# Performance work log

Measured on AMD Instinct MI355X. Metric: run time of the kernel, lower is better.

## Reference

```python
import jax, jax.numpy as jnp
import numpy as np

B, S, D, H = 2, 2048, 2048, 16
HD = D // H  # head_dim = 128


def setup_inputs() -> dict:
    key = jax.random.key(0)
    ks = jax.random.split(key, 9)
    s = 1.0 / np.sqrt(D)
    return {
        "x": jax.random.normal(ks[0], (B, S, D), jnp.float32),
        "Wq": jax.random.normal(ks[1], (D, D), jnp.float32) * s,
        "bq": jax.random.normal(ks[2], (D,), jnp.float32) * 0.02,
        "Wk": jax.random.normal(ks[3], (D, D), jnp.float32) * s,
        "bk": jax.random.normal(ks[4], (D,), jnp.float32) * 0.02,
        "Wv": jax.random.normal(ks[5], (D, D), jnp.float32) * s,
        "bv": jax.random.normal(ks[6], (D,), jnp.float32) * 0.02,
        "Wo": jax.random.normal(ks[7], (D, D), jnp.float32) * s,
        "bo": jax.random.normal(ks[8], (D,), jnp.float32) * 0.02,
    }


def reference(x, Wq, bq, Wk, bk, Wv, bv, Wo, bo):
    b, s, d = x.shape
    # nn.Linear: y = x @ W.T + b
    def split(t):
        # [b, s, d] -> [b, H, s, HD]
        return t.reshape(b, s, H, HD).transpose(0, 2, 1, 3)

    q = split(x @ Wq.T + bq)
    k = split(x @ Wk.T + bk)
    v = split(x @ Wv.T + bv)

    scale = jnp.asarray(HD, x.dtype) ** 0.5
    qk = jnp.einsum("bhqd,bhkd->bhqk", q, k) / scale  # [b, H, s, s]
    weights = jax.nn.softmax(qk, axis=-1)
    attn = jnp.einsum("bhqk,bhkd->bhqd", weights, v)  # [b, H, s, HD]

    merged = attn.transpose(0, 2, 1, 3).reshape(b, s, d)
    return merged @ Wo.T + bo
```

## Files before the change

### kernel.cpp

```cpp
#include <hip/hip_runtime.h>

typedef __bf16 bf16_t;
typedef bf16_t bf16x8 __attribute__((ext_vector_type(8)));
typedef bf16_t bf16x4 __attribute__((ext_vector_type(4)));
typedef float  f32x4  __attribute__((ext_vector_type(4)));

#define DDIM  2048
#define SEQ   2048
#define NH    16
#define HDIM  128
#define BATCH 2
#define MROWS (BATCH * SEQ)
#define XEL   ((size_t)MROWS * DDIM)
#define WEL   ((size_t)DDIM * DDIM)

__device__ __forceinline__ void async_ld16(const bf16_t* g, bf16_t* l) {
  __builtin_amdgcn_global_load_lds(
      (const __attribute__((address_space(1))) void*)g,
      (__attribute__((address_space(3))) void*)l, 16, 0, 0);
}

__global__ void cvt_all(const float* __restrict__ x,
                        const float* __restrict__ w0,
                        const float* __restrict__ w1,
                        const float* __restrict__ w2,
                        const float* __restrict__ w3,
                        bf16_t* __restrict__ ox, bf16_t* __restrict__ ow) {
  const size_t CX = XEL / 4;
  const size_t CW = WEL / 4;
  const size_t total = CX + 4 * CW;
  size_t c = (size_t)blockIdx.x * blockDim.x + threadIdx.x;
  const size_t stride = (size_t)gridDim.x * blockDim.x;
  for (; c < total; c += stride) {
    float4 v;
    bf16_t* outp;
    if (c < CX) {
      v = reinterpret_cast<const float4*>(x)[c];
      outp = ox + c * 4;
    } else {
      const size_t d = c - CX;
      const size_t seg = d >> 20;
      const float* w = seg == 0 ? w0 : seg == 1 ? w1 : seg == 2 ? w2 : w3;
      v = reinterpret_cast<const float4*>(w)[d & (CW - 1)];
      outp = ow + d * 4;
    }
    bf16x4 o;
    o[0] = (bf16_t)v.x; o[1] = (bf16_t)v.y;
    o[2] = (bf16_t)v.z; o[3] = (bf16_t)v.w;
    *reinterpret_cast<bf16x4*>(outp) = o;
  }
}

#define QMM(NF, BV)                                                           \
  __builtin_amdgcn_s_setprio(1);                                              \
  _Pragma("unroll") for (int mf = 0; mf < 4; ++mf) {                          \
    acc[mf][NF] = __builtin_amdgcn_mfma_f32_16x16x32_bf16(                    \
        a_[mf][0], BV[0], acc[mf][NF], 0, 0, 0);                              \
    acc[mf][NF] = __builtin_amdgcn_mfma_f32_16x16x32_bf16(                    \
        a_[mf][1], BV[1], acc[mf][NF], 0, 0, 0);                              \
  }                                                                           \
  __builtin_amdgcn_s_setprio(0);

#define LGKM(N)                                                               \
  asm volatile("s_waitcnt lgkmcnt(" #N ")" ::: "memory");                     \
  __builtin_amdgcn_sched_barrier(0);

__global__ __launch_bounds__(512, 2) void gemm_qkv(
    const bf16_t* __restrict__ Ax, const bf16_t* __restrict__ Wcat,
    const float* __restrict__ bq, const float* __restrict__ bk,
    const float* __restrict__ bv,
    bf16_t* __restrict__ QKVh, float qscale) {
  __shared__ __align__(16) bf16_t sA[2][2][128 * 64];
  __shared__ __align__(16) bf16_t sB[3][192 * 64];

  const int tid  = threadIdx.x;
  const int lane = tid & 63;
  const int w    = tid >> 6;
  const int wm   = w >> 1;
  const int wn   = w & 1;
  const int lg   = lane >> 4;
  const int lr   = lane & 15;

  const int bid = blockIdx.x;
  const int l   = (bid & 7) * 64 + (bid >> 3);
  const int tm  = l & 15;
  const int tn  = l >> 4;
  const int row0  = tm * 256;
  const int ncol0 = tn * 192;

  auto stA = [&](int buf, int ha, int kt) {
#pragma unroll
    for (int L = 0; L < 2; ++L) {
      const int c = L * 512 + tid, r = c >> 3, ch = c & 7;
      async_ld16(Ax + (size_t)(row0 + ha * 128 + r) * DDIM + kt * 64 +
                     ((ch ^ (r & 7)) * 8),
                 &sA[buf][ha][c * 8]);
    }
  };
  auto stB = [&](int buf, int kt) {
#pragma unroll
    for (int L = 0; L < 3; ++L) {
      const int c = L * 512 + tid, r = c >> 3, ch = c & 7;
      async_ld16(Wcat + (size_t)(ncol0 + r) * DDIM + kt * 64 +
                     ((ch ^ (r & 7)) * 8),
                 &sB[buf][c * 8]);
    }
  };
  auto ldA = [&](int buf, int mf, int k) {
    const int row = (wm & 1) * 64 + mf * 16 + lr;
    const int ch  = (k * 4 + lg) ^ (row & 7);
    return *reinterpret_cast<const bf16x8*>(
        &sA[buf][wm >> 1][row * 64 + ch * 8]);
  };
  auto ldB = [&](int buf, int nf, int k) {
    const int row = wn * 96 + nf * 16 + lr;
    const int ch  = (k * 4 + lg) ^ (row & 7);
    return *reinterpret_cast<const bf16x8*>(&sB[buf][row * 64 + ch * 8]);
  };

  f32x4 acc[4][6] = {};

  stA(0, 0, 0); stA(0, 1, 0);
  stB(0, 0);
  stB(1, 1);
  asm volatile("s_waitcnt vmcnt(3)" ::: "memory");
  __builtin_amdgcn_s_barrier();

  int bc = 0;
  for (int t = 0; t < 32; ++t) {
    const int p   = t & 1;
    const int pn  = p ^ 1;
    const int tn1 = (t + 1) & 31, tn2 = (t + 2) & 31;
    const int b2i = bc == 0 ? 2 : bc - 1;

    bf16x8 a_[4][2];
#pragma unroll
    for (int mf = 0; mf < 4; ++mf) {
      a_[mf][0] = ldA(p, mf, 0);
      a_[mf][1] = ldA(p, mf, 1);
    }
    bf16x8 b0[2], b1[2], b2[2], b3[2], b4[2], b5[2];
    b0[0] = ldB(bc, 0, 0); b0[1] = ldB(bc, 0, 1);
    b1[0] = ldB(bc, 1, 0); b1[1] = ldB(bc, 1, 1);
    b2[0] = ldB(bc, 2, 0); b2[1] = ldB(bc, 2, 1);
    __builtin_amdgcn_sched_barrier(0);
    stA(pn, 0, tn1); stA(pn, 1, tn1);
    stB(b2i, tn2);
    __builtin_amdgcn_sched_barrier(0);
    LGKM(4)
    QMM(0, b0)
    b3[0] = ldB(bc, 3, 0); b3[1] = ldB(bc, 3, 1);
    __builtin_amdgcn_sched_barrier(0);
    LGKM(4)
    QMM(1, b1)
    b4[0] = ldB(bc, 4, 0); b4[1] = ldB(bc, 4, 1);
    __builtin_amdgcn_sched_barrier(0);
    LGKM(4)
    QMM(2, b2)
    b5[0] = ldB(bc, 5, 0); b5[1] = ldB(bc, 5, 1);
    __builtin_amdgcn_sched_barrier(0);
    LGKM(4)
    QMM(3, b3)
    LGKM(2)
    QMM(4, b4)
    LGKM(0)
    QMM(5, b5)
    asm volatile("s_waitcnt vmcnt(3)" ::: "memory");
    __builtin_amdgcn_s_barrier();
    bc = bc == 2 ? 0 : bc + 1;
  }
  asm volatile("s_waitcnt vmcnt(0)" ::: "memory");

#pragma unroll
  for (int mf = 0; mf < 4; ++mf) {
    const int rr0 = row0 + wm * 64 + mf * 16 + lg * 4;
#pragma unroll
    for (int nf = 0; nf < 6; ++nf) {
      const int col = ncol0 + wn * 96 + nf * 16 + lr;
      const int mat = col >> 11;
      const int c2  = col & (DDIM - 1);
      const float bs = ((mat == 0) ? bq : (mat == 1) ? bk : bv)[c2];
      const float sc = (mat == 0) ? qscale : 1.0f;
      const int h = c2 >> 7, hd = c2 & (HDIM - 1);
      bf16_t* outb = QKVh + (size_t)mat * XEL;
#pragma unroll
      for (int r = 0; r < 4; ++r) {
        const int rr = rr0 + r;
        const int b = rr >> 11, s = rr & (SEQ - 1);
        outb[(((size_t)(b * NH + h)) * SEQ + s) * HDIM + hd] =
            (bf16_t)((acc[mf][nf][r] + bs) * sc);
      }
    }
  }
}

__global__ __launch_bounds__(512, 2) void gemm_bt(
    const bf16_t* __restrict__ A, const bf16_t* __restrict__ Bw,
    const float* __restrict__ bias, float* __restrict__ outp) {
  __shared__ __align__(16) bf16_t sA[2][2][128 * 64];
  __shared__ __align__(16) bf16_t sB[3][128 * 64];

  const int tid  = threadIdx.x;
  const int lane = tid & 63;
  const int w    = tid >> 6;
  const int wm   = w >> 1;
  const int wn   = w & 1;
  const int lg   = lane >> 4;
  const int lr   = lane & 15;

  const int bid = blockIdx.x;
  const int l   = (bid & 7) * 32 + (bid >> 3);
  const int tm  = l & 15;
  const int tn  = l >> 4;
  const int row0 = tm * 256;
  const int col0 = tn * 128;

  auto stA = [&](int buf, int ha, int kt) {
#pragma unroll
    for (int L = 0; L < 2; ++L) {
      const int c = L * 512 + tid, r = c >> 3, ch = c & 7;
      async_ld16(A + (size_t)(row0 + ha * 128 + r) * DDIM + kt * 64 +
                     ((ch ^ (r & 7)) * 8),
                 &sA[buf][ha][c * 8]);
    }
  };
  auto stB = [&](int buf, int kt) {
#pragma unroll
    for (int L = 0; L < 2; ++L) {
      const int c = L * 512 + tid, r = c >> 3, ch = c & 7;
      async_ld16(Bw + (size_t)(col0 + r) * DDIM + kt * 64 +
                     ((ch ^ (r & 7)) * 8),
                 &sB[buf][c * 8]);
    }
  };
  auto ldA = [&](int buf, int mf, int k) {
    const int row = (wm & 1) * 64 + mf * 16 + lr;
    const int ch  = (k * 4 + lg) ^ (row & 7);
    return *reinterpret_cast<const bf16x8*>(
        &sA[buf][wm >> 1][row * 64 + ch * 8]);
  };
  auto ldB = [&](int buf, int nf, int k) {
    const int row = wn * 64 + nf * 16 + lr;
    const int ch  = (k * 4 + lg) ^ (row & 7);
    return *reinterpret_cast<const bf16x8*>(&sB[buf][row * 64 + ch * 8]);
  };

  f32x4 acc[4][4] = {};

  stA(0, 0, 0); stA(0, 1, 0);
  stB(0, 0);
  stB(1, 1);
  asm volatile("s_waitcnt vmcnt(2)" ::: "memory");
  __builtin_amdgcn_s_barrier();

  int bc = 0;
  for (int t = 0; t < 32; ++t) {
    const int p   = t & 1;
    const int pn  = p ^ 1;
    const int tn1 = (t + 1) & 31, tn2 = (t + 2) & 31;
    const int b2i = bc == 0 ? 2 : bc - 1;

    bf16x8 a_[4][2];
#pragma unroll
    for (int mf = 0; mf < 4; ++mf) {
      a_[mf][0] = ldA(p, mf, 0);
      a_[mf][1] = ldA(p, mf, 1);
    }
    bf16x8 b0[2], b1[2], b2[2], b3[2];
    b0[0] = ldB(bc, 0, 0); b0[1] = ldB(bc, 0, 1);
    b1[0] = ldB(bc, 1, 0); b1[1] = ldB(bc, 1, 1);
    b2[0] = ldB(bc, 2, 0); b2[1] = ldB(bc, 2, 1);
    __builtin_amdgcn_sched_barrier(0);
    stA(pn, 0, tn1); stA(pn, 1, tn1);
    stB(b2i, tn2);
    __builtin_amdgcn_sched_barrier(0);
    LGKM(4)
    QMM(0, b0)
    b3[0] = ldB(bc, 3, 0); b3[1] = ldB(bc, 3, 1);
    __builtin_amdgcn_sched_barrier(0);
    LGKM(4)
    QMM(1, b1)
    LGKM(2)
    QMM(2, b2)
    LGKM(0)
    QMM(3, b3)
    asm volatile("s_waitcnt vmcnt(2)" ::: "memory");
    __builtin_amdgcn_s_barrier();
    bc = bc == 2 ? 0 : bc + 1;
  }
  asm volatile("s_waitcnt vmcnt(0)" ::: "memory");

#pragma unroll
  for (int mf = 0; mf < 4; ++mf) {
    const int row = row0 + wm * 64 + mf * 16 + lg * 4;
#pragma unroll
    for (int nf = 0; nf < 4; ++nf) {
      const int col = col0 + wn * 64 + nf * 16 + lr;
      const float bs = bias[col];
#pragma unroll
      for (int r = 0; r < 4; ++r)
        outp[(size_t)(row + r) * DDIM + col] = acc[mf][nf][r] + bs;
    }
  }
}

__global__ __launch_bounds__(256) void transpose_v(
    const bf16_t* __restrict__ Vp, bf16_t* __restrict__ Vt) {
  __shared__ __align__(16) bf16_t tt[64][72];
  const int bh = blockIdx.z;
  const int s0 = blockIdx.x * 64;
  const int d0 = blockIdx.y * 64;
  const int t  = threadIdx.x;
#pragma unroll
  for (int c = 0; c < 2; ++c) {
    const int r   = (c * 256 + t) >> 3;
    const int col = (t & 7) * 8;
    bf16x8 v = *reinterpret_cast<const bf16x8*>(
        Vp + ((size_t)bh * SEQ + s0 + r) * HDIM + d0 + col);
    *reinterpret_cast<bf16x8*>(&tt[r][col]) = v;
  }
  __syncthreads();
#pragma unroll
  for (int c = 0; c < 2; ++c) {
    const int dr = (c * 256 + t) >> 3;
    const int sc = (t & 7) * 8;
    bf16x8 o;
#pragma unroll
    for (int i = 0; i < 8; ++i) o[i] = tt[sc + i][dr];
    *reinterpret_cast<bf16x8*>(
        Vt + ((size_t)bh * HDIM + d0 + dr) * SEQ + s0 + sc) = o;
  }
}

__global__ __launch_bounds__(256) void attn_fwd(
    const bf16_t* __restrict__ Q, const bf16_t* __restrict__ K,
    const bf16_t* __restrict__ Vt, bf16_t* __restrict__ out) {
  __shared__ __align__(16) bf16_t sK[64 * 128];
  __shared__ __align__(16) bf16_t sV[128 * 64];
  __shared__ __align__(16) bf16_t sP[4][32][72];

  const int tid  = threadIdx.x;
  const int lane = tid & 63;
  const int w    = tid >> 6;
  const int lg   = lane >> 4;
  const int lr   = lane & 15;

  const int bid     = blockIdx.x;
  const int logical = (bid & 7) * 64 + (bid >> 3);
  const int bh      = logical >> 4;
  const int q0      = (logical & 15) * 128;
  const int qw      = q0 + w * 32;

  const bf16_t* Kb = K  + (size_t)bh * SEQ * HDIM;
  const bf16_t* Vb = Vt + (size_t)bh * HDIM * SEQ;

  bf16x8 qf[2][4];
#pragma unroll
  for (int mf = 0; mf < 2; ++mf) {
    const bf16_t* qbase = Q + ((size_t)bh * SEQ + qw + mf * 16 + lr) * HDIM;
#pragma unroll
    for (int kc = 0; kc < 4; ++kc)
      qf[mf][kc] = *reinterpret_cast<const bf16x8*>(qbase + kc * 32 + lg * 8);
  }

  bf16x8 onesf;
#pragma unroll
  for (int i = 0; i < 8; ++i) onesf[i] = (bf16_t)1.0f;

  f32x4 o[2][8] = {};
  f32x4 o1[2] = {};

  for (int kv0 = 0; kv0 < SEQ; kv0 += 64) {
    __syncthreads();
#pragma unroll
    for (int p = 0; p < 4; ++p) {
      const int slot = p * 256 + tid;
      const int kr = slot >> 4, kc = slot & 15;
      async_ld16(Kb + ((size_t)(kv0 + kr)) * HDIM + ((kc ^ (kr & 7)) * 8),
                 sK + slot * 8);
      const int vr = slot >> 3, vc = slot & 7;
      async_ld16(Vb + (size_t)vr * SEQ + kv0 + ((vc ^ (vr & 7)) * 8),
                 sV + slot * 8);
    }
    __syncthreads();

    f32x4 s[2][4] = {};
    __builtin_amdgcn_s_setprio(1);
#pragma unroll
    for (int kc = 0; kc < 4; ++kc) {
#pragma unroll
      for (int cb = 0; cb < 4; ++cb) {
        const int r  = cb * 16 + lr;
        const int ch = kc * 4 + lg;
        bf16x8 kf = *reinterpret_cast<const bf16x8*>(
            sK + r * 128 + ((ch ^ (r & 7)) * 8));
        s[0][cb] = __builtin_amdgcn_mfma_f32_16x16x32_bf16(qf[0][kc], kf, s[0][cb], 0, 0, 0);
        s[1][cb] = __builtin_amdgcn_mfma_f32_16x16x32_bf16(qf[1][kc], kf, s[1][cb], 0, 0, 0);
      }
    }
    __builtin_amdgcn_s_setprio(0);

#pragma unroll
    for (int mf = 0; mf < 2; ++mf)
#pragma unroll
      for (int r = 0; r < 4; ++r)
#pragma unroll
        for (int cb = 0; cb < 4; ++cb) {
          const float p = __builtin_amdgcn_exp2f(s[mf][cb][r]);
          sP[w][mf * 16 + lg * 4 + r][cb * 16 + lr] = (bf16_t)p;
        }

    asm volatile("s_waitcnt lgkmcnt(0)" ::: "memory");

    __builtin_amdgcn_s_setprio(1);
#pragma unroll
    for (int ks = 0; ks < 2; ++ks) {
      bf16x8 pf0 = *reinterpret_cast<const bf16x8*>(&sP[w][lr][ks * 32 + lg * 8]);
      bf16x8 pf1 = *reinterpret_cast<const bf16x8*>(&sP[w][16 + lr][ks * 32 + lg * 8]);
      o1[0] = __builtin_amdgcn_mfma_f32_16x16x32_bf16(pf0, onesf, o1[0], 0, 0, 0);
      o1[1] = __builtin_amdgcn_mfma_f32_16x16x32_bf16(pf1, onesf, o1[1], 0, 0, 0);
#pragma unroll
      for (int ob = 0; ob < 8; ++ob) {
        const int r  = ob * 16 + lr;
        const int ch = ks * 4 + lg;
        bf16x8 vf = *reinterpret_cast<const bf16x8*>(
            sV + r * 64 + ((ch ^ (r & 7)) * 8));
        o[0][ob] = __builtin_amdgcn_mfma_f32_16x16x32_bf16(pf0, vf, o[0][ob], 0, 0, 0);
        o[1][ob] = __builtin_amdgcn_mfma_f32_16x16x32_bf16(pf1, vf, o[1][ob], 0, 0, 0);
      }
    }
    __builtin_amdgcn_s_setprio(0);
  }

  const int b = bh >> 4, h = bh & 15;
#pragma unroll
  for (int mf = 0; mf < 2; ++mf) {
#pragma unroll
    for (int r = 0; r < 4; ++r) {
      const float inv_l = 1.0f / o1[mf][r];
      const int row = qw + mf * 16 + lg * 4 + r;
      bf16_t* obase = out + ((size_t)b * SEQ + row) * DDIM + h * HDIM;
#pragma unroll
      for (int ob = 0; ob < 8; ++ob)
        obase[ob * 16 + lr] = (bf16_t)(o[mf][ob][r] * inv_l);
    }
  }
}

extern "C" void kernel_launch(void* const* d_in, const int* in_sizes, int n_in,
                              void* d_out, int out_size, void* d_ws,
                              size_t ws_size, hipStream_t stream) {
  const float* x  = (const float*)d_in[0];
  const float* Wq = (const float*)d_in[1];
  const float* bq = (const float*)d_in[2];
  const float* Wk = (const float*)d_in[3];
  const float* bk = (const float*)d_in[4];
  const float* Wv = (const float*)d_in[5];
  const float* bv = (const float*)d_in[6];
  const float* Wo = (const float*)d_in[7];
  const float* bo = (const float*)d_in[8];

  bf16_t* ws = (bf16_t*)d_ws;
  const size_t XE = XEL;
  const size_t WE = WEL;
  bf16_t* xb  = ws;
  bf16_t* wqb = ws + XE;
  bf16_t* wkb = wqb + WE;
  bf16_t* wvb = wkb + WE;
  bf16_t* wob = wvb + WE;
  bf16_t* Qh  = wob + WE;
  bf16_t* Kh  = Qh + XE;
  bf16_t* Vh  = Kh + XE;
  bf16_t* Vt  = Vh + XE;
  bf16_t* merged = xb;

  cvt_all<<<2048, 256, 0, stream>>>(x, Wq, Wk, Wv, Wo, xb, wqb);

  const float qscale = 0.12751744520778695f;

  gemm_qkv<<<512, 512, 0, stream>>>(xb, wqb, bq, bk, bv, Qh, qscale);

  transpose_v<<<dim3(SEQ / 64, HDIM / 64, BATCH * NH), 256, 0, stream>>>(Vh, Vt);

  attn_fwd<<<512, 256, 0, stream>>>(Qh, Kh, Vt, merged);

  gemm_bt<<<256, 512, 0, stream>>>(merged, wob, bo, (float*)d_out);
}
```

Before: 259.9 us.

## Restructure QKV GEMM warp layout and double-buffer B with split LDS waits

Reworks the fused QKV projection GEMM so each of the 8 warps owns a 128x48 sub-tile (2x4 warp grid) instead of 64x96, loading eight A fragments and three B fragments per k-step. B shared-memory staging drops from triple to double buffering, and the main loop is unrolled into two halves with the global-to-LDS prefetches issued between MFMA phases and progressive lgkmcnt waits. The aim is to change the fragment reuse balance and overlap LDS reads with MFMA work. The cost is a second barrier per k-step, a shorter prefetch distance for B, and more registers held for A fragments.

```diff
diff --git a/kernel.cpp b/kernel.cpp
--- a/kernel.cpp
+++ b/kernel.cpp
@@ -51,6 +51,154 @@
   }
 }
 
+#define LGKM(N)                                                               \
+  asm volatile("s_waitcnt lgkmcnt(" #N ")" ::: "memory");                     \
+  __builtin_amdgcn_sched_barrier(0);
+
+__global__ __launch_bounds__(512, 2) void gemm_qkv(
+    const bf16_t* __restrict__ Ax, const bf16_t* __restrict__ Wcat,
+    const float* __restrict__ bq, const float* __restrict__ bk,
+    const float* __restrict__ bv,
+    bf16_t* __restrict__ QKVh, float qscale) {
+  __shared__ __align__(16) bf16_t sA[2][2][128 * 64];
+  __shared__ __align__(16) bf16_t sB[2][192 * 64];
+
+  const int tid  = threadIdx.x;
+  const int lane = tid & 63;
+  const int w    = tid >> 6;
+  const int wm   = w >> 2;
+  const int wn   = w & 3;
+  const int lg   = lane >> 4;
+  const int lr   = lane & 15;
+
+  const int bid = blockIdx.x;
+  const int l   = (bid & 7) * 64 + (bid >> 3);
+  const int tm  = l & 15;
+  const int tn  = l >> 4;
+  const int row0  = tm * 256;
+  const int ncol0 = tn * 192;
+
+  auto stA = [&](int buf, int ha, int kt) {
+#pragma unroll
+    for (int L = 0; L < 2; ++L) {
+      const int c = L * 512 + tid, r = c >> 3, ch = c & 7;
+      async_ld16(Ax + (size_t)(row0 + ha * 128 + r) * DDIM + kt * 64 +
+                     ((ch ^ (r & 7)) * 8),
+                 &sA[buf][ha][c * 8]);
+    }
+  };
+  auto stB = [&](int buf, int kt) {
+#pragma unroll
+    for (int L = 0; L < 3; ++L) {
+      const int c = L * 512 + tid, r = c >> 3, ch = c & 7;
+      async_ld16(Wcat + (size_t)(ncol0 + r) * DDIM + kt * 64 +
+                     ((ch ^ (r & 7)) * 8),
+                 &sB[buf][c * 8]);
+    }
+  };
+  auto ldA = [&](int buf, int mf, int k) {
+    const int row = mf * 16 + lr;
+    const int ch  = (k * 4 + lg) ^ (row & 7);
+    return *reinterpret_cast<const bf16x8*>(&sA[buf][wm][row * 64 + ch * 8]);
+  };
+  auto ldB = [&](int buf, int nf, int k) {
+    const int row = wn * 48 + nf * 16 + lr;
+    const int ch  = (k * 4 + lg) ^ (row & 7);
+    return *reinterpret_cast<const bf16x8*>(&sB[buf][row * 64 + ch * 8]);
+  };
+
+  f32x4  acc[8][3] = {};
+  bf16x8 a[8][2];
+  bf16x8 bfr[3][2];
+
+#define MFMA_PH(Q)                                                            \
+  __builtin_amdgcn_s_setprio(1);                                              \
+  _Pragma("unroll") for (int k = 0; k < 2; ++k) {                             \
+    _Pragma("unroll") for (int nf = 0; nf < 3; ++nf) {                        \
+      acc[2 * (Q)][nf] = __builtin_amdgcn_mfma_f32_16x16x32_bf16(             \
+          a[2 * (Q)][k], bfr[nf][k], acc[2 * (Q)][nf], 0, 0, 0);              \
+      acc[2 * (Q) + 1][nf] = __builtin_amdgcn_mfma_f32_16x16x32_bf16(         \
+          a[2 * (Q) + 1][k], bfr[nf][k], acc[2 * (Q) + 1][nf], 0, 0, 0);      \
+    }                                                                         \
+  }                                                                           \
+  __builtin_amdgcn_s_setprio(0);
+
+#define HALF(BUF, ST1, ST2)                                                   \
+  {                                                                           \
+       \
+    a[0][0] = ldA(BUF, 0, 0); a[0][1] = ldA(BUF, 0, 1);                       \
+    a[1][0] = ldA(BUF, 1, 0); a[1][1] = ldA(BUF, 1, 1);                       \
+    _Pragma("unroll") for (int nf = 0; nf < 3; ++nf) {                        \
+      bfr[nf][0] = ldB(BUF, nf, 0); bfr[nf][1] = ldB(BUF, nf, 1);             \
+    }                                                                         \
+    __builtin_amdgcn_sched_barrier(0);                                        \
+    a[2][0] = ldA(BUF, 2, 0); a[2][1] = ldA(BUF, 2, 1);                       \
+    a[3][0] = ldA(BUF, 3, 0); a[3][1] = ldA(BUF, 3, 1);                       \
+    __builtin_amdgcn_sched_barrier(0);                                        \
+    a[4][0] = ldA(BUF, 4, 0); a[4][1] = ldA(BUF, 4, 1);                       \
+    a[5][0] = ldA(BUF, 5, 0); a[5][1] = ldA(BUF, 5, 1);                       \
+    __builtin_amdgcn_sched_barrier(0);                                        \
+    a[6][0] = ldA(BUF, 6, 0); a[6][1] = ldA(BUF, 6, 1);                       \
+    a[7][0] = ldA(BUF, 7, 0); a[7][1] = ldA(BUF, 7, 1);                       \
+    ST1;                                                                      \
+    asm volatile("s_waitcnt lgkmcnt(12)" ::: "memory");                       \
+    __builtin_amdgcn_sched_barrier(0);                                        \
+    __builtin_amdgcn_s_barrier();                                             \
+    MFMA_PH(0)                                                                \
+    ST2;                                                                      \
+    asm volatile("s_waitcnt lgkmcnt(8)" ::: "memory");                        \
+    __builtin_amdgcn_sched_barrier(0);                                        \
+    MFMA_PH(1)                                                                \
+    asm volatile("s_waitcnt lgkmcnt(4)" ::: "memory");                        \
+    __builtin_amdgcn_sched_barrier(0);                                        \
+    MFMA_PH(2)                                                                \
+    asm volatile("s_waitcnt lgkmcnt(0)" ::: "memory");                        \
+    __builtin_amdgcn_sched_barrier(0);                                        \
+    MFMA_PH(3)                                                                \
+    asm volatile("s_waitcnt vmcnt(3)" ::: "memory");                          \
+    __builtin_amdgcn_s_barrier();                                             \
+  }
+
+  stA(0, 0, 0); stA(0, 1, 0);
+  stB(0, 0);
+  stB(1, 1);
+  asm volatile("s_waitcnt vmcnt(3)" ::: "memory");
+  __builtin_amdgcn_s_barrier();
+
+  for (int i = 0; i < 16; ++i) {
+    const int t1 = (2 * i + 1) & 31;
+    const int t2 = (2 * i + 2) & 31;
+    const int t3 = (2 * i + 3) & 31;
+    HALF(0, { stA(1, 0, t1); stA(1, 1, t1); }, { stB(0, t2); })
+    HALF(1, { stA(0, 0, t2); stA(0, 1, t2); }, { stB(1, t3); })
+  }
+#undef HALF
+#undef MFMA_PH
+  asm volatile("s_waitcnt vmcnt(0)" ::: "memory");
+
+#pragma unroll
+  for (int mf = 0; mf < 8; ++mf) {
+    const int rr0 = row0 + wm * 128 + mf * 16 + lg * 4;
+#pragma unroll
+    for (int nf = 0; nf < 3; ++nf) {
+      const int col = ncol0 + wn * 48 + nf * 16 + lr;
+      const int mat = col >> 11;
+      const int c2  = col & (DDIM - 1);
+      const float bs = ((mat == 0) ? bq : (mat == 1) ? bk : bv)[c2];
+      const float sc = (mat == 0) ? qscale : 1.0f;
+      const int h = c2 >> 7, hd = c2 & (HDIM - 1);
+      bf16_t* outb = QKVh + (size_t)mat * XEL;
+#pragma unroll
+      for (int r = 0; r < 4; ++r) {
+        const int rr = rr0 + r;
+        const int b = rr >> 11, s = rr & (SEQ - 1);
+        outb[(((size_t)(b * NH + h)) * SEQ + s) * HDIM + hd] =
+            (bf16_t)((acc[mf][nf][r] + bs) * sc);
+      }
+    }
+  }
+}
+
 #define QMM(NF, BV)                                                           \
   __builtin_amdgcn_s_setprio(1);                                              \
   _Pragma("unroll") for (int mf = 0; mf < 4; ++mf) {                          \
@@ -60,139 +208,6 @@
         a_[mf][1], BV[1], acc[mf][NF], 0, 0, 0);                              \
   }                                                                           \
   __builtin_amdgcn_s_setprio(0);
-
-#define LGKM(N)                                                               \
-  asm volatile("s_waitcnt lgkmcnt(" #N ")" ::: "memory");                     \
-  __builtin_amdgcn_sched_barrier(0);
-
-__global__ __launch_bounds__(512, 2) void gemm_qkv(
-    const bf16_t* __restrict__ Ax, const bf16_t* __restrict__ Wcat,
-    const float* __restrict__ bq, const float* __restrict__ bk,
-    const float* __restrict__ bv,
-    bf16_t* __restrict__ QKVh, float qscale) {
-  __shared__ __align__(16) bf16_t sA[2][2][128 * 64];
-  __shared__ __align__(16) bf16_t sB[3][192 * 64];
-
-  const int tid  = threadIdx.x;
-  const int lane = tid & 63;
-  const int w    = tid >> 6;
-  const int wm   = w >> 1;
-  const int wn   = w & 1;
-  const int lg   = lane >> 4;
-  const int lr   = lane & 15;
-
-  const int bid = blockIdx.x;
-  const int l   = (bid & 7) * 64 + (bid >> 3);
-  const int tm  = l & 15;
-  const int tn  = l >> 4;
-  const int row0  = tm * 256;
-  const int ncol0 = tn * 192;
-
-  auto stA = [&](int buf, int ha, int kt) {
-#pragma unroll
-    for (int L = 0; L < 2; ++L) {
-      const int c = L * 512 + tid, r = c >> 3, ch = c & 7;
-      async_ld16(Ax + (size_t)(row0 + ha * 128 + r) * DDIM + kt * 64 +
-                     ((ch ^ (r & 7)) * 8),
-                 &sA[buf][ha][c * 8]);
-    }
-  };
-  auto stB = [&](int buf, int kt) {
-#pragma unroll
-    for (int L = 0; L < 3; ++L) {
-      const int c = L * 512 + tid, r = c >> 3, ch = c & 7;
-      async_ld16(Wcat + (size_t)(ncol0 + r) * DDIM + kt * 64 +
-                     ((ch ^ (r & 7)) * 8),
-                 &sB[buf][c * 8]);
-    }
-  };
-  auto ldA = [&](int buf, int mf, int k) {
-    const int row = (wm & 1) * 64 + mf * 16 + lr;
-    const int ch  = (k * 4 + lg) ^ (row & 7);
-    return *reinterpret_cast<const bf16x8*>(
-        &sA[buf][wm >> 1][row * 64 + ch * 8]);
-  };
-  auto ldB = [&](int buf, int nf, int k) {
-    const int row = wn * 96 + nf * 16 + lr;
-    const int ch  = (k * 4 + lg) ^ (row & 7);
-    return *reinterpret_cast<const bf16x8*>(&sB[buf][row * 64 + ch * 8]);
-  };
-
-  f32x4 acc[4][6] = {};
-
-  stA(0, 0, 0); stA(0, 1, 0);
-  stB(0, 0);
-  stB(1, 1);
-  asm volatile("s_waitcnt vmcnt(3)" ::: "memory");
-  __builtin_amdgcn_s_barrier();
-
-  int bc = 0;
-  for (int t = 0; t < 32; ++t) {
-    const int p   = t & 1;
-    const int pn  = p ^ 1;
-    const int tn1 = (t + 1) & 31, tn2 = (t + 2) & 31;
-    const int b2i = bc == 0 ? 2 : bc - 1;
-
-    bf16x8 a_[4][2];
-#pragma unroll
-    for (int mf = 0; mf < 4; ++mf) {
-      a_[mf][0] = ldA(p, mf, 0);
-      a_[mf][1] = ldA(p, mf, 1);
-    }
-    bf16x8 b0[2], b1[2], b2[2], b3[2], b4[2], b5[2];
-    b0[0] = ldB(bc, 0, 0); b0[1] = ldB(bc, 0, 1);
-    b1[0] = ldB(bc, 1, 0); b1[1] = ldB(bc, 1, 1);
-    b2[0] = ldB(bc, 2, 0); b2[1] = ldB(bc, 2, 1);
-    __builtin_amdgcn_sched_barrier(0);
-    stA(pn, 0, tn1); stA(pn, 1, tn1);
-    stB(b2i, tn2);
-    __builtin_amdgcn_sched_barrier(0);
-    LGKM(4)
-    QMM(0, b0)
-    b3[0] = ldB(bc, 3, 0); b3[1] = ldB(bc, 3, 1);
-    __builtin_amdgcn_sched_barrier(0);
-    LGKM(4)
-    QMM(1, b1)
-    b4[0] = ldB(bc, 4, 0); b4[1] = ldB(bc, 4, 1);
-    __builtin_amdgcn_sched_barrier(0);
-    LGKM(4)
-    QMM(2, b2)
-    b5[0] = ldB(bc, 5, 0); b5[1] = ldB(bc, 5, 1);
-    __builtin_amdgcn_sched_barrier(0);
-    LGKM(4)
-    QMM(3, b3)
-    LGKM(2)
-    QMM(4, b4)
-    LGKM(0)
-    QMM(5, b5)
-    asm volatile("s_waitcnt vmcnt(3)" ::: "memory");
-    __builtin_amdgcn_s_barrier();
-    bc = bc == 2 ? 0 : bc + 1;
-  }
-  asm volatile("s_waitcnt vmcnt(0)" ::: "memory");
-
-#pragma unroll
-  for (int mf = 0; mf < 4; ++mf) {
-    const int rr0 = row0 + wm * 64 + mf * 16 + lg * 4;
-#pragma unroll
-    for (int nf = 0; nf < 6; ++nf) {
-      const int col = ncol0 + wn * 96 + nf * 16 + lr;
-      const int mat = col >> 11;
-      const int c2  = col & (DDIM - 1);
-      const float bs = ((mat == 0) ? bq : (mat == 1) ? bk : bv)[c2];
-      const float sc = (mat == 0) ? qscale : 1.0f;
-      const int h = c2 >> 7, hd = c2 & (HDIM - 1);
-      bf16_t* outb = QKVh + (size_t)mat * XEL;
-#pragma unroll
-      for (int r = 0; r < 4; ++r) {
-        const int rr = rr0 + r;
-        const int b = rr >> 11, s = rr & (SEQ - 1);
-        outb[(((size_t)(b * NH + h)) * SEQ + s) * HDIM + hd] =
-            (bf16_t)((acc[mf][nf][r] + bs) * sc);
-      }
-    }
-  }
-}
 
 __global__ __launch_bounds__(512, 2) void gemm_bt(
     const bf16_t* __restrict__ A, const bf16_t* __restrict__ Bw,
```

Result: faster. 246.5 us, median of 2 (-5.1%).
